# Performance work log

Measured on AMD Instinct MI355X. Metric: run time of the kernel, lower is better.

## Reference

```python
import jax, jax.numpy as jnp
import numpy as np

D_ATT = 1024
N_HEADS = 16
D_HEAD = D_ATT // N_HEADS


def _xavier(key, shape, scale):
    # xavier_uniform for Linear(d, d): limit = sqrt(6/(fan_in+fan_out))
    limit = float(np.sqrt(6.0 / (shape[0] + shape[1])))
    return jax.random.uniform(key, shape, jnp.float32, -limit, limit) * scale


def setup_inputs() -> dict:
    key = jax.random.key(0)
    ks = jax.random.split(key, 7)
    B, Lt, Ls = 2, 2048, 2048
    s = 1.0 / np.sqrt(D_ATT)
    return {
        "x_target": jax.random.normal(ks[0], (B, Lt, D_ATT), jnp.float32),
        "x_source": jax.random.normal(ks[1], (B, Ls, D_ATT), jnp.float32),
        "Wq": _xavier(ks[2], (D_ATT, D_ATT), s),  # torch Linear weight [out, in]
        "Wk": _xavier(ks[3], (D_ATT, D_ATT), s),
        "Wv": _xavier(ks[4], (D_ATT, D_ATT), s),
        "Wo": _xavier(ks[5], (D_ATT, D_ATT), 1.0),
        "bo": jax.random.uniform(ks[6], (D_ATT,), jnp.float32, -s, s),
    }


def reference(x_target, x_source, Wq, Wk, Wv, Wo, bo):
    B, Lt, _ = x_target.shape
    Ls = x_source.shape[1]
    H, Dh = N_HEADS, D_HEAD
    # projections (torch Linear: x @ W^T); RoPE defaults to identity
    Q = (x_target @ Wq.T).reshape(B, Lt, H, Dh)  # [B, Lt, H, Dh]
    K = (x_source @ Wk.T).reshape(B, Ls, H, Dh)
    V = (x_source @ Wv.T).reshape(B, Ls, H, Dh)
    scores = jnp.einsum("bthd,bshd->bhts", Q, K) / np.sqrt(Dh)
    attn = jax.nn.softmax(scores, axis=-1)
    out = jnp.einsum("bhts,bshd->bthd", attn, V).reshape(B, Lt, H * Dh)
    return out @ Wo.T + bo  # dropout p=0 -> identity
```

## Files before the change

### kernel.cpp

```cpp
#include <hip/hip_runtime.h>
#include <hip/hip_bf16.h>

typedef short bf16x8 __attribute__((ext_vector_type(8)));
typedef float f32x4 __attribute__((ext_vector_type(4)));

#define LDP 72

__device__ __forceinline__ float bf2f(ushort u) {
    union { unsigned int i; float f; } v; v.i = ((unsigned int)u) << 16; return v.f;
}
__device__ __forceinline__ ushort f2bf(float f) {
    union { float f; unsigned int i; } v; v.f = f;
    unsigned int x = v.i;
    x += 0x7fffu + ((x >> 16) & 1u);
    return (ushort)(x >> 16);
}

#define MFMA(a, b, c) __builtin_amdgcn_mfma_f32_16x16x32_bf16(a, b, c, 0, 0, 0)

#define WAIT_BARRIER(N) asm volatile("s_waitcnt vmcnt(" #N ")\n\ts_barrier" ::: "memory")

__device__ __forceinline__ void gld_lds16(const ushort* g, ushort* l) {
    __builtin_amdgcn_global_load_lds(
        (const __attribute__((address_space(1))) unsigned int*)g,
        (__attribute__((address_space(3))) unsigned int*)l, 16, 0, 0);
}

#define WS_XT 0
#define WS_XS 4194304
#define WS_WQ 8388608
#define WS_WK 9437184
#define WS_WV 10485760
#define WS_WO 11534336
#define WS_QH 12582912
#define WS_KH 16777216
#define WS_VT 20971520
#define WS_AO 0

__global__ __launch_bounds__(256) void cast_bf16(
    const float* __restrict__ s0, const float* __restrict__ s1,
    const float* __restrict__ s2, const float* __restrict__ s3,
    const float* __restrict__ s4, const float* __restrict__ s5,
    ushort* __restrict__ ws)
{
    const int seg = blockIdx.y;
    const float* src = seg == 0 ? s0 : seg == 1 ? s1 : seg == 2 ? s2
                     : seg == 3 ? s3 : seg == 4 ? s4 : s5;
    const size_t off = seg == 0 ? WS_XT : seg == 1 ? WS_XS : seg == 2 ? WS_WQ
                     : seg == 3 ? WS_WK : seg == 4 ? WS_WV : (size_t)WS_WO;
    const int n4 = (seg < 2) ? 1048576 : 262144;
    ushort* d = ws + off;
    for (int i = blockIdx.x * 256 + threadIdx.x; i < n4; i += gridDim.x * 256) {
        float4 f = ((const float4*)src)[i];
        ushort4 u;
        u.x = f2bf(f.x); u.y = f2bf(f.y); u.z = f2bf(f.z); u.w = f2bf(f.w);
        ((ushort4*)d)[i] = u;
    }
}

__global__ __launch_bounds__(256) void gemm128(
    const ushort* __restrict__ xtb, const ushort* __restrict__ xsb,
    const ushort* __restrict__ wqb, const ushort* __restrict__ wkb,
    const ushort* __restrict__ wvb,
    ushort* __restrict__ qh, ushort* __restrict__ kh, ushort* __restrict__ vt)
{
    __shared__ __align__(16) ushort SM[24576];

    const int mode = blockIdx.z;
    const ushort* Ap = (mode == 0) ? xtb : xsb;
    const ushort* Wp = (mode == 0) ? wqb : (mode == 1 ? wkb : wvb);

    const int tid  = threadIdx.x;
    const int wave = tid >> 6, lane = tid & 63;
    const int quad = lane >> 4, lidx = lane & 15;
    const int wm = wave >> 1, wn = wave & 1;
    const int m0 = blockIdx.y * 128, n0 = blockIdx.x * 128;

    const int slr = lane >> 2, scb = lane & 3;
    auto stage = [&](int k0, int bufi) {
        ushort* Asb = SM + bufi * 4096;
        ushort* Bsb = SM + 12288 + bufi * 4096;
#pragma unroll
        for (int i2 = 0; i2 < 2; ++i2) {
            const int i = wave + i2 * 4;
            const int r = i * 16 + slr;
            gld_lds16(Ap + (size_t)(m0 + r) * 1024 + k0 + scb * 8, Asb + i * 512);
            gld_lds16(Wp + (size_t)(n0 + r) * 1024 + k0 + scb * 8, Bsb + i * 512);
        }
    };

    f32x4 acc[4][4] = {};
    stage(0, 0);
    stage(32, 1);

    for (int kt = 0; kt < 32; ++kt) {
        const int cur = kt % 3;
        WAIT_BARRIER(4);
        stage(((kt + 2) & 31) * 32, (kt + 2) % 3);
        const ushort* Asb = SM + cur * 4096;
        const ushort* Bsb = SM + 12288 + cur * 4096;
        bf16x8 af[4], bfr[4];
#pragma unroll
        for (int i = 0; i < 4; ++i) {
            af[i]  = *(const bf16x8*)(Asb + (wm * 64 + i * 16 + lidx) * 32 + quad * 8);
            bfr[i] = *(const bf16x8*)(Bsb + (wn * 64 + i * 16 + lidx) * 32 + quad * 8);
        }
#pragma unroll
        for (int mi = 0; mi < 4; ++mi)
#pragma unroll
            for (int ni = 0; ni < 4; ++ni)
                acc[mi][ni] = MFMA(af[mi], bfr[ni], acc[mi][ni]);
    }
    __syncthreads();

    ushort* scr = SM + wave * 4096;

    if (mode == 2) {
#pragma unroll
        for (int mi = 0; mi < 4; ++mi)
#pragma unroll
            for (int ni = 0; ni < 4; ++ni)
#pragma unroll
                for (int r = 0; r < 4; ++r) {
                    const int dl = ni * 16 + lidx;
                    const int tl = mi * 16 + quad * 4 + r;
                    const int col = (((tl >> 3) ^ (dl & 7)) << 3) | (tl & 7);
                    scr[dl * 64 + col] = f2bf(acc[mi][ni][r]);
                }
        asm volatile("s_waitcnt lgkmcnt(0)" ::: "memory");
        const int hh = (n0 + wn * 64) >> 6;
        const int bb = m0 >> 11;
        const int t0 = (m0 + wm * 64) & 2047;
        ushort* Vtp = vt + (size_t)(bb * 16 + hh) * 64 * 2048;
#pragma unroll
        for (int ii = 0; ii < 8; ++ii) {
            const int dl = ii * 8 + (lane >> 3);
            const int tb = lane & 7;
            uint4 vd = *(const uint4*)(scr + dl * 64 + ((tb ^ (dl & 7)) << 3));
            *(uint4*)(Vtp + (size_t)dl * 2048 + t0 + tb * 8) = vd;
        }
        return;
    }

#pragma unroll
    for (int mi = 0; mi < 4; ++mi)
#pragma unroll
        for (int ni = 0; ni < 4; ++ni)
#pragma unroll
            for (int r = 0; r < 4; ++r) {
                const int tl = mi * 16 + quad * 4 + r;
                const int dl = ni * 16 + lidx;
                const int col = (((dl >> 3) ^ (tl & 7)) << 3) | (dl & 7);
                scr[tl * 64 + col] = f2bf(acc[mi][ni][r]);
            }
    asm volatile("s_waitcnt lgkmcnt(0)" ::: "memory");
    {
        ushort* dst = (mode == 0) ? qh : kh;
        const int hh = (n0 + wn * 64) >> 6;
        const int bb = m0 >> 11;
        const int tbase = (m0 + wm * 64) & 2047;
        ushort* Hp = dst + (size_t)(bb * 16 + hh) * 2048 * 64;
#pragma unroll
        for (int ii = 0; ii < 8; ++ii) {
            const int tl = ii * 8 + (lane >> 3);
            const int c  = lane & 7;
            uint4 vd = *(const uint4*)(scr + tl * 64 + ((c ^ (tl & 7)) << 3));
            *(uint4*)(Hp + (size_t)(tbase + tl) * 64 + c * 8) = vd;
        }
    }
}

__global__ __launch_bounds__(256) void gemm_out(
    const ushort* __restrict__ aob, const ushort* __restrict__ wob,
    const float* __restrict__ bias, float* __restrict__ outf)
{
    __shared__ __align__(16) ushort SM[18432];

    const int tid  = threadIdx.x;
    const int wave = tid >> 6, lane = tid & 63;
    const int quad = lane >> 4, lidx = lane & 15;
    const int m0 = blockIdx.y * 128, n0 = blockIdx.x * 64;

    const int slr = lane >> 2, scb = lane & 3;
    auto stage = [&](int k0, int bufi) {
        ushort* Asb = SM + bufi * 4096;
        ushort* Bsb = SM + 12288 + bufi * 2048;
#pragma unroll
        for (int i2 = 0; i2 < 2; ++i2) {
            const int i = wave * 2 + i2;
            gld_lds16(aob + (size_t)(m0 + i * 16 + slr) * 1024 + k0 + scb * 8,
                      Asb + i * 512);
        }
        gld_lds16(wob + (size_t)(n0 + wave * 16 + slr) * 1024 + k0 + scb * 8,
                  Bsb + wave * 512);
    };

    f32x4 acc[2][4] = {};
    stage(0, 0);
    stage(32, 1);

    for (int kt = 0; kt < 32; ++kt) {
        const int cur = kt % 3;
        WAIT_BARRIER(3);
        stage(((kt + 2) & 31) * 32, (kt + 2) % 3);
        const ushort* Asb = SM + cur * 4096;
        const ushort* Bsb = SM + 12288 + cur * 2048;
        bf16x8 af[2], bfr[4];
#pragma unroll
        for (int i = 0; i < 2; ++i)
            af[i] = *(const bf16x8*)(Asb + (wave * 32 + i * 16 + lidx) * 32 + quad * 8);
#pragma unroll
        for (int i = 0; i < 4; ++i)
            bfr[i] = *(const bf16x8*)(Bsb + (i * 16 + lidx) * 32 + quad * 8);
#pragma unroll
        for (int mi = 0; mi < 2; ++mi)
#pragma unroll
            for (int ni = 0; ni < 4; ++ni)
                acc[mi][ni] = MFMA(af[mi], bfr[ni], acc[mi][ni]);
    }

#pragma unroll
    for (int mi = 0; mi < 2; ++mi)
#pragma unroll
        for (int ni = 0; ni < 4; ++ni)
#pragma unroll
            for (int r = 0; r < 4; ++r) {
                const int m = m0 + wave * 32 + mi * 16 + quad * 4 + r;
                const int n = n0 + ni * 16 + lidx;
                outf[(size_t)m * 1024 + n] = acc[mi][ni][r] + bias[n];
            }
}

__global__ __launch_bounds__(512) void flash_attn(
    const ushort* __restrict__ Qh, const ushort* __restrict__ Kh,
    const ushort* __restrict__ Vt, ushort* __restrict__ AO)
{
    __shared__ __align__(16) ushort Kb[2][4096];
    __shared__ __align__(16) ushort Vb[2][4096];
    __shared__ __align__(16) ushort P[8][16][LDP];

    const int tid  = threadIdx.x;
    const int wave = tid >> 6, lane = tid & 63;
    const int quad = lane >> 4, lidx = lane & 15;
    const int bh = blockIdx.y;
    const int b = bh >> 4, h = bh & 15;
    const int qbase = blockIdx.x * 128 + wave * 16;

    const ushort* Qp = Qh + (size_t)bh * 2048 * 64;
    const ushort* Kp = Kh + (size_t)bh * 2048 * 64;
    const ushort* Vp = Vt + (size_t)bh * 64 * 2048;

    bf16x8 q0, q1;
    {
        const ushort* qr = Qp + (size_t)(qbase + lidx) * 64 + quad * 8;
        union { ushort u[8]; uint4 v; } t0, t1;
        t0.v = *(const uint4*)qr;
        t1.v = *(const uint4*)(qr + 32);
#pragma unroll
        for (int i = 0; i < 8; ++i) {
            ((short*)&q0)[i] = (short)f2bf(bf2f(t0.u[i]) * 0.18033688f);
            ((short*)&q1)[i] = (short)f2bf(bf2f(t1.u[i]) * 0.18033688f);
        }
    }

    auto stage = [&](int s0, int bufi) {
        const int slot = wave * 64 + lane;
        const int r  = slot >> 3;
        const int bb = slot & 7;
        const int gb = bb ^ (r & 7);
        gld_lds16(Kp + (size_t)(s0 + r) * 64 + gb * 8, &Kb[bufi][wave * 512]);
        gld_lds16(Vp + (size_t)r * 2048 + s0 + gb * 8, &Vb[bufi][wave * 512]);
    };

    float lsum[4] = {};
    f32x4 o[4] = {};

    stage(0, 0);
    __syncthreads();

    for (int j = 0; j < 32; ++j) {
        const int cur = j & 1;
        stage(((j + 1) & 31) * 64, cur ^ 1);

        f32x4 s[4] = {};
#pragma unroll
        for (int n0 = 0; n0 < 4; ++n0) {
            const int row = n0 * 16 + lidx;
            bf16x8 k0 = *(const bf16x8*)&Kb[cur][row * 64 + ((quad ^ (row & 7)) * 8)];
            bf16x8 k1 = *(const bf16x8*)&Kb[cur][row * 64 + (((4 + quad) ^ (row & 7)) * 8)];
            s[n0] = MFMA(q0, k0, s[n0]);
            s[n0] = MFMA(q1, k1, s[n0]);
        }

#pragma unroll
        for (int n0 = 0; n0 < 4; ++n0)
#pragma unroll
            for (int r = 0; r < 4; ++r) {
                const float p = __builtin_amdgcn_exp2f(s[n0][r]);
                lsum[r] += p;
                P[wave][quad * 4 + r][n0 * 16 + lidx] = f2bf(p);
            }
        asm volatile("s_waitcnt lgkmcnt(0)" ::: "memory");
        bf16x8 p0 = *(const bf16x8*)&P[wave][lidx][quad * 8];
        bf16x8 p1 = *(const bf16x8*)&P[wave][lidx][32 + quad * 8];

#pragma unroll
        for (int n0 = 0; n0 < 4; ++n0) {
            const int d = n0 * 16 + lidx;
            bf16x8 v0 = *(const bf16x8*)&Vb[cur][d * 64 + ((quad ^ (d & 7)) * 8)];
            bf16x8 v1 = *(const bf16x8*)&Vb[cur][d * 64 + (((4 + quad) ^ (d & 7)) * 8)];
            o[n0] = MFMA(p0, v0, o[n0]);
            o[n0] = MFMA(p1, v1, o[n0]);
        }
        __syncthreads();
    }

#pragma unroll
    for (int r = 0; r < 4; ++r) {
        float v = lsum[r];
        v += __shfl_xor(v, 1);
        v += __shfl_xor(v, 2);
        v += __shfl_xor(v, 4);
        v += __shfl_xor(v, 8);
        lsum[r] = v;
    }

#pragma unroll
    for (int n0 = 0; n0 < 4; ++n0)
#pragma unroll
        for (int r = 0; r < 4; ++r) {
            const int tt = qbase + quad * 4 + r;
            const int d  = n0 * 16 + lidx;
            AO[(size_t)(b * 2048 + tt) * 1024 + h * 64 + d] =
                f2bf(o[n0][r] / lsum[r]);
        }
}

extern "C" void kernel_launch(void* const* d_in, const int* in_sizes, int n_in,
                              void* d_out, int out_size, void* d_ws, size_t ws_size,
                              hipStream_t stream) {
    const float* xt = (const float*)d_in[0];
    const float* xs = (const float*)d_in[1];
    const float* Wq = (const float*)d_in[2];
    const float* Wk = (const float*)d_in[3];
    const float* Wv = (const float*)d_in[4];
    const float* Wo = (const float*)d_in[5];
    const float* bo = (const float*)d_in[6];
    float* out = (float*)d_out;

    ushort* ws = (ushort*)d_ws;

    cast_bf16<<<dim3(1024, 6, 1), 256, 0, stream>>>(xt, xs, Wq, Wk, Wv, Wo, ws);

    gemm128<<<dim3(8, 32, 3), 256, 0, stream>>>(
        ws + WS_XT, ws + WS_XS, ws + WS_WQ, ws + WS_WK, ws + WS_WV,
        ws + WS_QH, ws + WS_KH, ws + WS_VT);

    flash_attn<<<dim3(16, 32, 1), 512, 0, stream>>>(
        ws + WS_QH, ws + WS_KH, ws + WS_VT, ws + WS_AO);

    gemm_out<<<dim3(16, 32, 1), 256, 0, stream>>>(
        ws + WS_AO, ws + WS_WO, bo, out);
}
```

Baseline: 207.9 us.

## Process two query row-blocks per wave in flash attention with 256 threads

Halves the block to 4 waves, each now covering 32 query rows, so every K/V fragment read from LDS feeds two MFMAs. Q and K are swapped in the score MFMA, producing transposed scores, so P can be written as packed bf16 pairs (v_cvt_pk_bf16_f32) in 8-byte stores instead of scalar stores. The row-sum reduction and normalization are restructured to match, using a reciprocal multiply. Each wave holds more accumulators, which raises register pressure and may lower occupancy.

```diff
diff --git a/kernel.cpp b/kernel.cpp
--- a/kernel.cpp
+++ b/kernel.cpp
@@ -231,49 +231,55 @@
             }
 }
 
-__global__ __launch_bounds__(512) void flash_attn(
+__global__ __launch_bounds__(256) void flash_attn(
     const ushort* __restrict__ Qh, const ushort* __restrict__ Kh,
     const ushort* __restrict__ Vt, ushort* __restrict__ AO)
 {
     __shared__ __align__(16) ushort Kb[2][4096];
     __shared__ __align__(16) ushort Vb[2][4096];
-    __shared__ __align__(16) ushort P[8][16][LDP];
+    __shared__ __align__(16) ushort P[4][32][LDP];
 
     const int tid  = threadIdx.x;
     const int wave = tid >> 6, lane = tid & 63;
     const int quad = lane >> 4, lidx = lane & 15;
     const int bh = blockIdx.y;
     const int b = bh >> 4, h = bh & 15;
-    const int qbase = blockIdx.x * 128 + wave * 16;
+    const int qbase = blockIdx.x * 128 + wave * 32;
 
     const ushort* Qp = Qh + (size_t)bh * 2048 * 64;
     const ushort* Kp = Kh + (size_t)bh * 2048 * 64;
     const ushort* Vp = Vt + (size_t)bh * 64 * 2048;
 
-    bf16x8 q0, q1;
-    {
-        const ushort* qr = Qp + (size_t)(qbase + lidx) * 64 + quad * 8;
+    bf16x8 q[2][2];
+#pragma unroll
+    for (int rb = 0; rb < 2; ++rb) {
+        const ushort* qr = Qp + (size_t)(qbase + rb * 16 + lidx) * 64 + quad * 8;
         union { ushort u[8]; uint4 v; } t0, t1;
         t0.v = *(const uint4*)qr;
         t1.v = *(const uint4*)(qr + 32);
 #pragma unroll
         for (int i = 0; i < 8; ++i) {
-            ((short*)&q0)[i] = (short)f2bf(bf2f(t0.u[i]) * 0.18033688f);
-            ((short*)&q1)[i] = (short)f2bf(bf2f(t1.u[i]) * 0.18033688f);
+            ((short*)&q[rb][0])[i] = (short)f2bf(bf2f(t0.u[i]) * 0.18033688f);
+            ((short*)&q[rb][1])[i] = (short)f2bf(bf2f(t1.u[i]) * 0.18033688f);
         }
     }
 
     auto stage = [&](int s0, int bufi) {
-        const int slot = wave * 64 + lane;
-        const int r  = slot >> 3;
-        const int bb = slot & 7;
-        const int gb = bb ^ (r & 7);
-        gld_lds16(Kp + (size_t)(s0 + r) * 64 + gb * 8, &Kb[bufi][wave * 512]);
-        gld_lds16(Vp + (size_t)r * 2048 + s0 + gb * 8, &Vb[bufi][wave * 512]);
+#pragma unroll
+        for (int i = 0; i < 2; ++i) {
+            const int slot = i * 256 + wave * 64 + lane;
+            const int r  = slot >> 3;
+            const int bb = slot & 7;
+            const int gb = bb ^ (r & 7);
+            gld_lds16(Kp + (size_t)(s0 + r) * 64 + gb * 8,
+                      &Kb[bufi][i * 2048 + wave * 512]);
+            gld_lds16(Vp + (size_t)r * 2048 + s0 + gb * 8,
+                      &Vb[bufi][i * 2048 + wave * 512]);
+        }
     };
 
-    float lsum[4] = {};
-    f32x4 o[4] = {};
+    float lsum[2] = {};
+    f32x4 o[2][4] = {};
 
     stage(0, 0);
     __syncthreads();
@@ -282,58 +288,83 @@
         const int cur = j & 1;
         stage(((j + 1) & 31) * 64, cur ^ 1);
 
-        f32x4 s[4] = {};
+        f32x4 s[2][4] = {};
 #pragma unroll
         for (int n0 = 0; n0 < 4; ++n0) {
             const int row = n0 * 16 + lidx;
-            bf16x8 k0 = *(const bf16x8*)&Kb[cur][row * 64 + ((quad ^ (row & 7)) * 8)];
-            bf16x8 k1 = *(const bf16x8*)&Kb[cur][row * 64 + (((4 + quad) ^ (row & 7)) * 8)];
-            s[n0] = MFMA(q0, k0, s[n0]);
-            s[n0] = MFMA(q1, k1, s[n0]);
-        }
-
-#pragma unroll
-        for (int n0 = 0; n0 < 4; ++n0)
-#pragma unroll
-            for (int r = 0; r < 4; ++r) {
-                const float p = __builtin_amdgcn_exp2f(s[n0][r]);
-                lsum[r] += p;
-                P[wave][quad * 4 + r][n0 * 16 + lidx] = f2bf(p);
+            bf16x8 kA = *(const bf16x8*)&Kb[cur][row * 64 + ((quad ^ (row & 7)) * 8)];
+            bf16x8 kB = *(const bf16x8*)&Kb[cur][row * 64 + (((4 + quad) ^ (row & 7)) * 8)];
+#pragma unroll
+            for (int rb = 0; rb < 2; ++rb) {
+                s[rb][n0] = MFMA(kA, q[rb][0], s[rb][n0]);
+                s[rb][n0] = MFMA(kB, q[rb][1], s[rb][n0]);
+            }
+        }
+
+#pragma unroll
+        for (int rb = 0; rb < 2; ++rb)
+#pragma unroll
+            for (int n0 = 0; n0 < 4; ++n0) {
+                float p0 = __builtin_amdgcn_exp2f(s[rb][n0][0]);
+                float p1 = __builtin_amdgcn_exp2f(s[rb][n0][1]);
+                float p2 = __builtin_amdgcn_exp2f(s[rb][n0][2]);
+                float p3 = __builtin_amdgcn_exp2f(s[rb][n0][3]);
+                lsum[rb] += (p0 + p1) + (p2 + p3);
+                uint u0, u1;
+                asm("v_cvt_pk_bf16_f32 %0, %1, %2" : "=v"(u0) : "v"(p0), "v"(p1));
+                asm("v_cvt_pk_bf16_f32 %0, %1, %2" : "=v"(u1) : "v"(p2), "v"(p3));
+                union { uint u[2]; uint2 v; } pw;
+                pw.u[0] = u0; pw.u[1] = u1;
+                *(uint2*)&P[wave][rb * 16 + lidx][n0 * 16 + quad * 4] = pw.v;
             }
         asm volatile("s_waitcnt lgkmcnt(0)" ::: "memory");
-        bf16x8 p0 = *(const bf16x8*)&P[wave][lidx][quad * 8];
-        bf16x8 p1 = *(const bf16x8*)&P[wave][lidx][32 + quad * 8];
+
+        bf16x8 pA[2], pB[2];
+#pragma unroll
+        for (int rb = 0; rb < 2; ++rb) {
+            pA[rb] = *(const bf16x8*)&P[wave][rb * 16 + lidx][quad * 8];
+            pB[rb] = *(const bf16x8*)&P[wave][rb * 16 + lidx][32 + quad * 8];
+        }
 
 #pragma unroll
         for (int n0 = 0; n0 < 4; ++n0) {
             const int d = n0 * 16 + lidx;
             bf16x8 v0 = *(const bf16x8*)&Vb[cur][d * 64 + ((quad ^ (d & 7)) * 8)];
             bf16x8 v1 = *(const bf16x8*)&Vb[cur][d * 64 + (((4 + quad) ^ (d & 7)) * 8)];
-            o[n0] = MFMA(p0, v0, o[n0]);
-            o[n0] = MFMA(p1, v1, o[n0]);
+#pragma unroll
+            for (int rb = 0; rb < 2; ++rb) {
+                o[rb][n0] = MFMA(pA[rb], v0, o[rb][n0]);
+                o[rb][n0] = MFMA(pB[rb], v1, o[rb][n0]);
+            }
         }
         __syncthreads();
     }
 
 #pragma unroll
-    for (int r = 0; r < 4; ++r) {
-        float v = lsum[r];
-        v += __shfl_xor(v, 1);
-        v += __shfl_xor(v, 2);
-        v += __shfl_xor(v, 4);
-        v += __shfl_xor(v, 8);
-        lsum[r] = v;
-    }
-
-#pragma unroll
-    for (int n0 = 0; n0 < 4; ++n0)
-#pragma unroll
-        for (int r = 0; r < 4; ++r) {
-            const int tt = qbase + quad * 4 + r;
-            const int d  = n0 * 16 + lidx;
-            AO[(size_t)(b * 2048 + tt) * 1024 + h * 64 + d] =
-                f2bf(o[n0][r] / lsum[r]);
-        }
+    for (int rb = 0; rb < 2; ++rb) {
+        float v = lsum[rb];
+        v += __shfl_xor(v, 16);
+        v += __shfl_xor(v, 32);
+        lsum[rb] = v;
+    }
+    float rs[2][4];
+#pragma unroll
+    for (int rb = 0; rb < 2; ++rb)
+#pragma unroll
+        for (int r = 0; r < 4; ++r)
+            rs[rb][r] = 1.0f / __shfl(lsum[rb], quad * 4 + r);
+
+#pragma unroll
+    for (int rb = 0; rb < 2; ++rb)
+#pragma unroll
+        for (int n0 = 0; n0 < 4; ++n0)
+#pragma unroll
+            for (int r = 0; r < 4; ++r) {
+                const int tt = qbase + rb * 16 + quad * 4 + r;
+                const int d  = n0 * 16 + lidx;
+                AO[(size_t)(b * 2048 + tt) * 1024 + h * 64 + d] =
+                    f2bf(o[rb][n0][r] * rs[rb][r]);
+            }
 }
 
 extern "C" void kernel_launch(void* const* d_in, const int* in_sizes, int n_in,
@@ -356,7 +387,7 @@
         ws + WS_XT, ws + WS_XS, ws + WS_WQ, ws + WS_WK, ws + WS_WV,
         ws + WS_QH, ws + WS_KH, ws + WS_VT);
 
-    flash_attn<<<dim3(16, 32, 1), 512, 0, stream>>>(
+    flash_attn<<<dim3(16, 32, 1), 256, 0, stream>>>(
         ws + WS_QH, ws + WS_KH, ws + WS_VT, ws + WS_AO);
 
     gemm_out<<<dim3(16, 32, 1), 256, 0, stream>>>(
```

After: 205.4 us. Within noise of the previous version (-1.2%).

## Triple-buffer K/V tiles and transpose QK MFMA to simplify P staging

Applied to the files above, without the earlier changes.

Moves the flash-attention K/V staging from double to triple buffering with a vmcnt-based wait and barrier, so two tiles are in flight and the per-iteration trailing __syncthreads is gone. Swaps the QK^T MFMA operands so each lane holds scores for one query row, allowing packed bf16 conversion with v_cvt_pk_bf16_f32 and one 8-byte LDS store per score tile instead of scalar stores. V fragments are loaded before the softmax to overlap LDS latency, and the row sum becomes one scalar per lane reduced with fewer shuffles and applied as a reciprocal multiply. Costs extra LDS and register pressure, and depends on the vmcnt(2) count matching the two outstanding staged loads.

```diff
diff --git a/kernel.cpp b/kernel.cpp
--- a/kernel.cpp
+++ b/kernel.cpp
@@ -235,8 +235,8 @@
     const ushort* __restrict__ Qh, const ushort* __restrict__ Kh,
     const ushort* __restrict__ Vt, ushort* __restrict__ AO)
 {
-    __shared__ __align__(16) ushort Kb[2][4096];
-    __shared__ __align__(16) ushort Vb[2][4096];
+    __shared__ __align__(16) ushort Kb[3][4096];
+    __shared__ __align__(16) ushort Vb[3][4096];
     __shared__ __align__(16) ushort P[8][16][LDP];
 
     const int tid  = threadIdx.x;
@@ -272,58 +272,71 @@
         gld_lds16(Vp + (size_t)r * 2048 + s0 + gb * 8, &Vb[bufi][wave * 512]);
     };
 
-    float lsum[4] = {};
+    float lsum = 0.f;
     f32x4 o[4] = {};
 
     stage(0, 0);
-    __syncthreads();
+    stage(64, 1);
 
     for (int j = 0; j < 32; ++j) {
-        const int cur = j & 1;
-        stage(((j + 1) & 31) * 64, cur ^ 1);
+        const int cur = j % 3;
+        WAIT_BARRIER(2);
+        stage(((j + 2) & 31) * 64, (j + 2) % 3);
 
         f32x4 s[4] = {};
 #pragma unroll
         for (int n0 = 0; n0 < 4; ++n0) {
             const int row = n0 * 16 + lidx;
-            bf16x8 k0 = *(const bf16x8*)&Kb[cur][row * 64 + ((quad ^ (row & 7)) * 8)];
-            bf16x8 k1 = *(const bf16x8*)&Kb[cur][row * 64 + (((4 + quad) ^ (row & 7)) * 8)];
-            s[n0] = MFMA(q0, k0, s[n0]);
-            s[n0] = MFMA(q1, k1, s[n0]);
-        }
-
-#pragma unroll
-        for (int n0 = 0; n0 < 4; ++n0)
-#pragma unroll
-            for (int r = 0; r < 4; ++r) {
-                const float p = __builtin_amdgcn_exp2f(s[n0][r]);
-                lsum[r] += p;
-                P[wave][quad * 4 + r][n0 * 16 + lidx] = f2bf(p);
-            }
-        asm volatile("s_waitcnt lgkmcnt(0)" ::: "memory");
-        bf16x8 p0 = *(const bf16x8*)&P[wave][lidx][quad * 8];
-        bf16x8 p1 = *(const bf16x8*)&P[wave][lidx][32 + quad * 8];
-
+            bf16x8 kA = *(const bf16x8*)&Kb[cur][row * 64 + ((quad ^ (row & 7)) * 8)];
+            bf16x8 kB = *(const bf16x8*)&Kb[cur][row * 64 + (((4 + quad) ^ (row & 7)) * 8)];
+            s[n0] = MFMA(kA, q0, s[n0]);
+            s[n0] = MFMA(kB, q1, s[n0]);
+        }
+
+        bf16x8 v0[4], v1[4];
 #pragma unroll
         for (int n0 = 0; n0 < 4; ++n0) {
             const int d = n0 * 16 + lidx;
-            bf16x8 v0 = *(const bf16x8*)&Vb[cur][d * 64 + ((quad ^ (d & 7)) * 8)];
-            bf16x8 v1 = *(const bf16x8*)&Vb[cur][d * 64 + (((4 + quad) ^ (d & 7)) * 8)];
-            o[n0] = MFMA(p0, v0, o[n0]);
-            o[n0] = MFMA(p1, v1, o[n0]);
-        }
-        __syncthreads();
-    }
-
-#pragma unroll
-    for (int r = 0; r < 4; ++r) {
-        float v = lsum[r];
-        v += __shfl_xor(v, 1);
-        v += __shfl_xor(v, 2);
-        v += __shfl_xor(v, 4);
-        v += __shfl_xor(v, 8);
-        lsum[r] = v;
-    }
+            v0[n0] = *(const bf16x8*)&Vb[cur][d * 64 + ((quad ^ (d & 7)) * 8)];
+            v1[n0] = *(const bf16x8*)&Vb[cur][d * 64 + (((4 + quad) ^ (d & 7)) * 8)];
+        }
+
+#pragma unroll
+        for (int n0 = 0; n0 < 4; ++n0) {
+            float p0 = __builtin_amdgcn_exp2f(s[n0][0]);
+            float p1 = __builtin_amdgcn_exp2f(s[n0][1]);
+            float p2 = __builtin_amdgcn_exp2f(s[n0][2]);
+            float p3 = __builtin_amdgcn_exp2f(s[n0][3]);
+            lsum += (p0 + p1) + (p2 + p3);
+            uint u0, u1;
+            asm("v_cvt_pk_bf16_f32 %0, %1, %2" : "=v"(u0) : "v"(p0), "v"(p1));
+            asm("v_cvt_pk_bf16_f32 %0, %1, %2" : "=v"(u1) : "v"(p2), "v"(p3));
+            union { uint u[2]; uint2 v; } pw;
+            pw.u[0] = u0; pw.u[1] = u1;
+            *(uint2*)&P[wave][lidx][n0 * 16 + quad * 4] = pw.v;
+        }
+        asm volatile("s_waitcnt lgkmcnt(0)" ::: "memory");
+
+        bf16x8 pA = *(const bf16x8*)&P[wave][lidx][quad * 8];
+        bf16x8 pB = *(const bf16x8*)&P[wave][lidx][32 + quad * 8];
+
+#pragma unroll
+        for (int n0 = 0; n0 < 4; ++n0) {
+            o[n0] = MFMA(pA, v0[n0], o[n0]);
+            o[n0] = MFMA(pB, v1[n0], o[n0]);
+        }
+    }
+
+    {
+        float v = lsum;
+        v += __shfl_xor(v, 16);
+        v += __shfl_xor(v, 32);
+        lsum = v;
+    }
+    float rs[4];
+#pragma unroll
+    for (int r = 0; r < 4; ++r)
+        rs[r] = 1.0f / __shfl(lsum, quad * 4 + r);
 
 #pragma unroll
     for (int n0 = 0; n0 < 4; ++n0)
@@ -332,7 +345,7 @@
             const int tt = qbase + quad * 4 + r;
             const int d  = n0 * 16 + lidx;
             AO[(size_t)(b * 2048 + tt) * 1024 + h * 64 + d] =
-                f2bf(o[n0][r] / lsum[r]);
+                f2bf(o[n0][r] * rs[r]);
         }
 }
 
```

Measured after the change: 201.8 us. 1.03x faster.
